# Optimization experiments

Hardware: AMD Instinct MI355X
Metric: run time of the kernel (lower is better)

## Reference

```python
import jax, jax.numpy as jnp
import numpy as np


def _chamfer(x1, x2):
    # x1: [B,N,3], x2: [B,M,3]
    # squared pairwise distances via ||a||^2 + ||b||^2 - 2 a.b (fused, no [B,N,M,3] diff tensor)
    n1 = jnp.sum(x1 * x1, axis=-1)                     # [B,N]
    n2 = jnp.sum(x2 * x2, axis=-1)                     # [B,M]
    cross = jnp.einsum('bnd,bmd->bnm', x1, x2)         # [B,N,M]
    d = n1[:, :, None] + n2[:, None, :] - 2.0 * cross  # [B,N,M]
    d = jnp.maximum(d, 0.0)
    dist1 = jnp.min(d, axis=2)  # [B,N] nearest in x2 for each x1 point
    dist2 = jnp.min(d, axis=1)  # [B,M] nearest in x1 for each x2 point
    return dist1, dist2


def setup_inputs() -> dict:
    key = jax.random.key(0)
    k1, k2 = jax.random.split(key)
    B, N, M, D = 16, 4096, 4096, 3
    input1 = jax.random.normal(k1, (B, N, D), dtype=jnp.float32)
    input2 = jax.random.normal(k2, (B, M, D), dtype=jnp.float32)
    return {"input1": input1, "input2": input2}


def reference(input1, input2):
    return _chamfer(input1, input2)
```

## Files before the change

kernel.cpp:

```cpp
#include <hip/hip_runtime.h>


#define CB 16
#define CN 4096
#define CM 4096
#define WVS 8
#define QPW 16
#define QPB (WVS * QPW)
#define TPC 1024
#define NCH (CM / TPC)
#define NTT (TPC / 16)

typedef float f32x4 __attribute__((ext_vector_type(4)));
typedef float f32x2 __attribute__((ext_vector_type(2)));
typedef short bf16x8 __attribute__((ext_vector_type(8)));
typedef unsigned int u32;
typedef u32 u32x4 __attribute__((ext_vector_type(4)));

__device__ __forceinline__ u32 pack2(float a, float b) {
    return __builtin_amdgcn_perm(__float_as_uint(b), __float_as_uint(a),
                                 0x07060302u);
}
__device__ __forceinline__ float hi_f(float a) {
    return __uint_as_float(__float_as_uint(a) & 0xFFFF0000u);
}

__global__ __launch_bounds__(512, 8) void chamfer_mfma(
    const float* __restrict__ x1, const float* __restrict__ x2,
    float* __restrict__ out)
{
    const int dir   = blockIdx.z;
    const int b     = blockIdx.y;
    const int qtile = blockIdx.x;

    const float* __restrict__ qraw = (dir ? x2 : x1) + (size_t)b * CN * 3;
    const float* __restrict__ traw = (dir ? x1 : x2) + (size_t)b * CM * 3;
    float* __restrict__ o = out + (dir ? ((size_t)CB * CN + (size_t)b * CM)
                                       : ((size_t)b * CN)) + qtile * QPB;

    __shared__ u32x4 AI[NTT * 32];

    const int tid  = threadIdx.x;
    const int lane = tid & 63;
    const int wave = __builtin_amdgcn_readfirstlane(tid >> 6);
    const int col  = lane & 15;
    const int kb   = lane >> 4;
    const int lsel = lane & 31;

    bf16x8 bq;
    float nq;
    {
        const float* qp = qraw + (size_t)3 * (qtile * QPB + wave * QPW + col);
        float qx = qp[0], qy = qp[1], qz = qp[2];
        nq = fmaf(qx, qx, fmaf(qy, qy, qz * qz));
        float MX = -2.f * qx, MY = -2.f * qy, MZ = -2.f * qz;
        float mxl = MX - hi_f(MX);
        float myl = MY - hi_f(MY);
        float mzl = MZ - hi_f(MZ);
        u32x4 w;
        if (kb == 0)
            w = (u32x4){pack2(MX, MY), pack2(MZ, MX),
                        pack2(MY, MZ), pack2(mxl, myl)};
        else if (kb == 1)
            w = (u32x4){pack2(mzl, 1.0f), pack2(1.0f, 0.f), 0u, 0u};
        else
            w = (u32x4){0u, 0u, 0u, 0u};
        bq = __builtin_bit_cast(bf16x8, w);
    }

    float best0 = 1e30f, best1 = 1e30f;

    #pragma unroll 1
    for (int c = 0; c < NCH; ++c) {
        {
            const f32x2* rv = (const f32x2*)(traw + (size_t)(c * TPC + 2 * tid) * 3);
            f32x2 r0 = rv[0], r1 = rv[1], r2 = rv[2];
            const float tx[2] = {r0.x, r1.y};
            const float ty[2] = {r0.y, r2.x};
            const float tz[2] = {r1.x, r2.y};
            #pragma unroll
            for (int i = 0; i < 2; ++i) {
                float X = tx[i], Y = ty[i], Zc = tz[i];
                float xl = X - hi_f(X);
                float yl = Y - hi_f(Y);
                float zl = Zc - hi_f(Zc);
                float nt = fmaf(X, X, fmaf(Y, Y, Zc * Zc));
                float ntl = nt - hi_f(nt);
                const int r = 2 * tid + i;
                const int base = (r >> 4) * 32 + (r & 15);
                AI[base +  0] = (u32x4){pack2(X, Y), pack2(Zc, xl),
                                        pack2(yl, zl), pack2(X, Y)};
                AI[base + 16] = (u32x4){pack2(Zc, nt), pack2(ntl, 0.f),
                                        0u, 0u};
            }
        }
        __syncthreads();

        #pragma unroll 1
        for (int t = 0; t < NTT; t += 4) {
            #pragma unroll
            for (int u = 0; u < 4; ++u) {
                bf16x8 af = __builtin_bit_cast(bf16x8, AI[(t + u) * 32 + lsel]);
                f32x4 acc = __builtin_amdgcn_mfma_f32_16x16x32_bf16(
                    af, bq, (f32x4){0.f, 0.f, 0.f, 0.f}, 0, 0, 0);
                best0 = fminf(fminf(best0, acc.x), acc.y);
                best1 = fminf(fminf(best1, acc.z), acc.w);
            }
        }
        __syncthreads();
    }

    float v = fminf(best0, best1);
    v = fminf(v, __shfl_xor(v, 16));
    v = fminf(v, __shfl_xor(v, 32));
    if (kb == 0)
        o[wave * QPW + col] = fmaxf(v + nq, 0.f);
}

extern "C" void kernel_launch(void* const* d_in, const int* in_sizes, int n_in,
                              void* d_out, int out_size, void* d_ws, size_t ws_size,
                              hipStream_t stream) {
    const float* x1 = (const float*)d_in[0];
    const float* x2 = (const float*)d_in[1];
    float* out = (float*)d_out;

    chamfer_mfma<<<dim3(32, CB, 2), 512, 0, stream>>>(x1, x2, out);
}
```

Measured before the change: 82.35 us.

## Switch to 32x32x8 bf16 MFMA with whole target set staged once in LDS

Replaces the 16x16x32 MFMA formulation with 32x32x8 MFMA and packs the distance expansion into K=8. The query-side coefficients are RNE-rounded to a single bf16 term, which drops their low-part correction. All 4096 target points are staged into LDS once, removing the per-chunk barriers. Each wave now handles 32 queries, so the grid is halved. Dropping the query low parts lowers precision, and the larger LDS footprint (64KB) reduces occupancy.

Measured after the change: 68.44 us, median of 2. 16.9% less time.

```diff
diff --git a/kernel.cpp b/kernel.cpp
--- a/kernel.cpp
+++ b/kernel.cpp
@@ -5,17 +5,14 @@
 #define CN 4096
 #define CM 4096
 #define WVS 8
-#define QPW 16
+#define QPW 32
 #define QPB (WVS * QPW)
-#define TPC 1024
-#define NCH (CM / TPC)
-#define NTT (TPC / 16)
+#define NTT (CM / 32)
 
-typedef float f32x4 __attribute__((ext_vector_type(4)));
-typedef float f32x2 __attribute__((ext_vector_type(2)));
-typedef short bf16x8 __attribute__((ext_vector_type(8)));
+typedef float f32x16 __attribute__((ext_vector_type(16)));
+typedef short bf16x4 __attribute__((ext_vector_type(4)));
 typedef unsigned int u32;
-typedef u32 u32x4 __attribute__((ext_vector_type(4)));
+typedef u32 u32x2 __attribute__((ext_vector_type(2)));
 
 __device__ __forceinline__ u32 pack2(float a, float b) {
     return __builtin_amdgcn_perm(__float_as_uint(b), __float_as_uint(a),
@@ -24,8 +21,13 @@
 __device__ __forceinline__ float hi_f(float a) {
     return __uint_as_float(__float_as_uint(a) & 0xFFFF0000u);
 }
+__device__ __forceinline__ float rne_bf(float f) {
+    u32 u = __float_as_uint(f);
+    u32 r = (u + 0x7FFFu + ((u >> 16) & 1u)) & 0xFFFF0000u;
+    return __uint_as_float(r);
+}
 
-__global__ __launch_bounds__(512, 8) void chamfer_mfma(
+__global__ __launch_bounds__(512, 4) void chamfer_mfma(
     const float* __restrict__ x1, const float* __restrict__ x2,
     float* __restrict__ out)
 {
@@ -38,82 +40,69 @@
     float* __restrict__ o = out + (dir ? ((size_t)CB * CN + (size_t)b * CM)
                                        : ((size_t)b * CN)) + qtile * QPB;
 
-    __shared__ u32x4 AI[NTT * 32];
+    __shared__ u32x2 AI[NTT * 64];
 
     const int tid  = threadIdx.x;
     const int lane = tid & 63;
     const int wave = __builtin_amdgcn_readfirstlane(tid >> 6);
-    const int col  = lane & 15;
-    const int kb   = lane >> 4;
-    const int lsel = lane & 31;
+    const int col  = lane & 31;
+    const int h    = lane >> 5;
 
-    bf16x8 bq;
+    #pragma unroll
+    for (int j = 0; j < 8; ++j) {
+        const int r = 512 * j + tid;
+        const float* p = traw + 3 * r;
+        float X = p[0], Y = p[1], Zc = p[2];
+        float xl = X  - hi_f(X);
+        float yl = Y  - hi_f(Y);
+        float zl = Zc - hi_f(Zc);
+        float nt  = fmaf(X, X, fmaf(Y, Y, Zc * Zc));
+        float ntl = nt - hi_f(nt);
+        const int e = (r >> 5) * 64 + (r & 31);
+        AI[e]      = (u32x2){pack2(X, Y),   pack2(Zc, xl)};
+        AI[e + 32] = (u32x2){pack2(yl, zl), pack2(nt, ntl)};
+    }
+
     float nq;
+    bf16x4 bq;
     {
         const float* qp = qraw + (size_t)3 * (qtile * QPB + wave * QPW + col);
         float qx = qp[0], qy = qp[1], qz = qp[2];
         nq = fmaf(qx, qx, fmaf(qy, qy, qz * qz));
-        float MX = -2.f * qx, MY = -2.f * qy, MZ = -2.f * qz;
-        float mxl = MX - hi_f(MX);
-        float myl = MY - hi_f(MY);
-        float mzl = MZ - hi_f(MZ);
-        u32x4 w;
-        if (kb == 0)
-            w = (u32x4){pack2(MX, MY), pack2(MZ, MX),
-                        pack2(MY, MZ), pack2(mxl, myl)};
-        else if (kb == 1)
-            w = (u32x4){pack2(mzl, 1.0f), pack2(1.0f, 0.f), 0u, 0u};
+        float mx = rne_bf(-2.f * qx);
+        float my = rne_bf(-2.f * qy);
+        float mz = rne_bf(-2.f * qz);
+        u32x2 w;
+        if (h == 0)
+            w = (u32x2){pack2(mx, my), pack2(mz, mx)};
         else
-            w = (u32x4){0u, 0u, 0u, 0u};
-        bq = __builtin_bit_cast(bf16x8, w);
+            w = (u32x2){pack2(my, mz), pack2(1.0f, 1.0f)};
+        bq = __builtin_bit_cast(bf16x4, w);
     }
 
-    float best0 = 1e30f, best1 = 1e30f;
+    float best = 1e30f;
+    __syncthreads();
 
     #pragma unroll 1
-    for (int c = 0; c < NCH; ++c) {
-        {
-            const f32x2* rv = (const f32x2*)(traw + (size_t)(c * TPC + 2 * tid) * 3);
-            f32x2 r0 = rv[0], r1 = rv[1], r2 = rv[2];
-            const float tx[2] = {r0.x, r1.y};
-            const float ty[2] = {r0.y, r2.x};
-            const float tz[2] = {r1.x, r2.y};
-            #pragma unroll
-            for (int i = 0; i < 2; ++i) {
-                float X = tx[i], Y = ty[i], Zc = tz[i];
-                float xl = X - hi_f(X);
-                float yl = Y - hi_f(Y);
-                float zl = Zc - hi_f(Zc);
-                float nt = fmaf(X, X, fmaf(Y, Y, Zc * Zc));
-                float ntl = nt - hi_f(nt);
-                const int r = 2 * tid + i;
-                const int base = (r >> 4) * 32 + (r & 15);
-                AI[base +  0] = (u32x4){pack2(X, Y), pack2(Zc, xl),
-                                        pack2(yl, zl), pack2(X, Y)};
-                AI[base + 16] = (u32x4){pack2(Zc, nt), pack2(ntl, 0.f),
-                                        0u, 0u};
-            }
+    for (int t = 0; t < NTT; t += 4) {
+        #pragma unroll
+        for (int u = 0; u < 4; ++u) {
+            bf16x4 af = __builtin_bit_cast(bf16x4, AI[(t + u) * 64 + lane]);
+            f32x16 acc = __builtin_amdgcn_mfma_f32_32x32x8bf16_1k(
+                af, bq, (f32x16)(0.f), 0, 0, 0);
+            float t0 = fminf(fminf(acc[0],  acc[1]),  acc[2]);
+            float t1 = fminf(fminf(acc[3],  acc[4]),  acc[5]);
+            float t2 = fminf(fminf(acc[6],  acc[7]),  acc[8]);
+            float t3 = fminf(fminf(acc[9],  acc[10]), acc[11]);
+            float t4 = fminf(fminf(acc[12], acc[13]), acc[14]);
+            float u0 = fminf(fminf(t0, t1), t2);
+            float u1 = fminf(fminf(t3, t4), acc[15]);
+            best = fminf(fminf(best, u0), u1);
         }
-        __syncthreads();
-
-        #pragma unroll 1
-        for (int t = 0; t < NTT; t += 4) {
-            #pragma unroll
-            for (int u = 0; u < 4; ++u) {
-                bf16x8 af = __builtin_bit_cast(bf16x8, AI[(t + u) * 32 + lsel]);
-                f32x4 acc = __builtin_amdgcn_mfma_f32_16x16x32_bf16(
-                    af, bq, (f32x4){0.f, 0.f, 0.f, 0.f}, 0, 0, 0);
-                best0 = fminf(fminf(best0, acc.x), acc.y);
-                best1 = fminf(fminf(best1, acc.z), acc.w);
-            }
-        }
-        __syncthreads();
     }
 
-    float v = fminf(best0, best1);
-    v = fminf(v, __shfl_xor(v, 16));
-    v = fminf(v, __shfl_xor(v, 32));
-    if (kb == 0)
+    float v = fminf(best, __shfl_xor(best, 32));
+    if (lane < 32)
         o[wave * QPW + col] = fmaxf(v + nq, 0.f);
 }
 
@@ -124,5 +113,5 @@
     const float* x2 = (const float*)d_in[1];
     float* out = (float*)d_out;
 
-    chamfer_mfma<<<dim3(32, CB, 2), 512, 0, stream>>>(x1, x2, out);
+    chamfer_mfma<<<dim3(16, CB, 2), 512, 0, stream>>>(x1, x2, out);
 }
```
